# Kernel tuning notes

Measured on AMD Instinct MI355X. Metric: run time of the kernel, lower is better.

Reference implementation:

```python
import jax, jax.numpy as jnp
import numpy as np

N = 8000          # num_nodes
DEG = 8           # avg out-degree of random road graph
B = 32            # batch size
INPUT_DIM = 2
UNITS = 64        # rnn_units
K = 2             # max_diffusion_step
NUM_SUPPORTS = 2  # dual_random_walk


def _spmm(rows, cols, vals, x):
    # sparse @ dense: y[r] += vals * x[c] for each coo entry (r, c)
    return jax.ops.segment_sum(vals[:, None] * x[cols], rows, num_segments=N)


def _gconv(inputs, state, supports, W, b):
    # Chebyshev-style diffusion conv, faithful to GCONV.forward layout
    Bsz = inputs.shape[0]
    x = jnp.concatenate([inputs.reshape(Bsz, N, -1), state.reshape(Bsz, N, -1)], axis=2)
    F = x.shape[2]                                   # input_dim + units
    x0 = jnp.transpose(x, (1, 2, 0)).reshape(N, F * Bsz)
    xs = [x0]
    for rows, cols, vals in supports:
        x1 = _spmm(rows, cols, vals, x0)
        xs.append(x1)
        xk2, xk1 = x0, x1
        for _ in range(2, K + 1):
            x2 = 2.0 * _spmm(rows, cols, vals, xk1) - xk2
            xs.append(x2)
            xk2, xk1 = xk1, x2
    M = len(xs)                                      # num_matrices = 2*K+1
    xc = jnp.stack(xs).reshape(M, N, F, Bsz)
    xc = jnp.transpose(xc, (3, 1, 2, 0)).reshape(Bsz * N, F * M)
    out = xc @ W + b
    return out.reshape(Bsz, N * W.shape[1])


def setup_inputs() -> dict:
    rng = np.random.default_rng(0)
    rows = np.repeat(np.arange(N, dtype=np.int32), DEG)
    cols = rng.integers(0, N, size=N * DEG).astype(np.int32)
    vals = rng.uniform(0.5, 1.5, size=N * DEG).astype(np.float32)
    # random-walk normalization: rw(A) = D^-1 A ; supports are rw(A).T and rw(A.T).T
    rsum = np.zeros(N, np.float32); np.add.at(rsum, rows, vals)
    csum = np.zeros(N, np.float32); np.add.at(csum, cols, vals)
    rinv = np.where(rsum > 0, 1.0 / np.maximum(rsum, 1e-12), 0.0).astype(np.float32)
    cinv = np.where(csum > 0, 1.0 / np.maximum(csum, 1e-12), 0.0).astype(np.float32)
    # support0 = (D^-1 A)^T: entry (cols[i], rows[i]) = vals[i] * rinv[rows[i]]
    s0_rows, s0_cols, s0_vals = cols, rows, (vals * rinv[rows]).astype(np.float32)
    # support1 = (D_T^-1 A^T)^T: entry (rows[i], cols[i]) = vals[i] * cinv[cols[i]]
    s1_rows, s1_cols, s1_vals = rows, cols, (vals * cinv[cols]).astype(np.float32)

    key = jax.random.key(0)
    k1, k2, k3, k4 = jax.random.split(key, 4)
    F = INPUT_DIM + UNITS
    M = NUM_SUPPORTS * K + 1
    xavier = lambda k, shape: jax.random.normal(k, shape, jnp.float32) * np.float32(np.sqrt(2.0 / (shape[0] + shape[1])))
    W_ru = xavier(k1, (F * M, 2 * UNITS))
    b_ru = jnp.ones((2 * UNITS,), jnp.float32)    # bias_start=1.0
    W_c = xavier(k2, (F * M, UNITS))
    b_c = jnp.zeros((UNITS,), jnp.float32)        # bias_start=0.0
    inputs = jax.random.normal(k3, (B, N * INPUT_DIM), jnp.float32)
    hx = jax.random.normal(k4, (B, N * UNITS), jnp.float32)
    return {
        "inputs": inputs, "hx": hx,
        "W_ru": W_ru, "b_ru": b_ru, "W_c": W_c, "b_c": b_c,
        "s0_rows": jnp.asarray(s0_rows), "s0_cols": jnp.asarray(s0_cols), "s0_vals": jnp.asarray(s0_vals),
        "s1_rows": jnp.asarray(s1_rows), "s1_cols": jnp.asarray(s1_cols), "s1_vals": jnp.asarray(s1_vals),
    }


def reference(inputs, hx, W_ru, b_ru, W_c, b_c,
              s0_rows, s0_cols, s0_vals, s1_rows, s1_cols, s1_vals):
    supports = [(s0_rows, s0_cols, s0_vals), (s1_rows, s1_cols, s1_vals)]
    value = jax.nn.sigmoid(_gconv(inputs, hx, supports, W_ru, b_ru))
    value = value.reshape(-1, N, 2 * UNITS)
    r = value[..., :UNITS].reshape(-1, N * UNITS)
    u = value[..., UNITS:].reshape(-1, N * UNITS)
    c = jnp.tanh(_gconv(inputs, r * hx, supports, W_c, b_c))
    return u * hx + (1.0 - u) * c
```

## Files before the change

kernel.cpp:

```cpp
#include <hip/hip_runtime.h>
#include <stdint.h>

typedef unsigned short u16;
typedef unsigned int   u32;

typedef __attribute__((ext_vector_type(8))) short bf16x8;
typedef __attribute__((ext_vector_type(4))) float f32x4;

#define NNODES 8000
#define BSZ    32
#define UNITS  64
#define EDG    64000
#define ROWCH  288
#define ROWU16 2304
#define KLIN   480
#define HXROW  512000
#define INROW  16000
#define NROW   18432000
#define NSTEPS 15

__device__ __forceinline__ u32 f2bf(float f){
    u32 u = __float_as_uint(f);
    return (u + 0x7FFFu + ((u >> 16) & 1u)) >> 16;
}
__device__ __forceinline__ float bfu(u16 s){ return __uint_as_float(((u32)s) << 16); }
__device__ __forceinline__ float lo16(u32 u){ return __uint_as_float(u << 16); }
__device__ __forceinline__ float hi16(u32 u){ return __uint_as_float(u & 0xFFFF0000u); }
__device__ __forceinline__ float sigm(float x){ return 1.f / (1.f + __expf(-x)); }

#define GLDS(gsrc, ldst) \
    __builtin_amdgcn_global_load_lds((const __attribute__((address_space(1))) void*)(gsrc), \
                                     (__attribute__((address_space(3))) void*)(ldst), 16, 0, 0)

__global__ void hist_k(const int* __restrict__ rows, int* __restrict__ counts){
    int e = blockIdx.x * 256 + threadIdx.x;
    if (e < EDG) atomicAdd(&counts[rows[e]], 1);
}

__global__ __launch_bounds__(256) void scan_k(const int* __restrict__ counts,
                                              int* __restrict__ row_ptr,
                                              int* __restrict__ cursor){
    __shared__ int part[256];
    int t = threadIdx.x;
    int s = 0;
    for (int i = 0; i < 32; ++i){ int r = t*32 + i; if (r < NNODES) s += counts[r]; }
    part[t] = s;
    __syncthreads();
    if (t == 0){
        int run = 0;
        for (int i = 0; i < 256; ++i){ int v = part[i]; part[i] = run; run += v; }
    }
    __syncthreads();
    int run = part[t];
    for (int i = 0; i < 32; ++i){
        int r = t*32 + i;
        if (r < NNODES){ row_ptr[r] = run; cursor[r] = run; run += counts[r]; }
    }
    if (t == 255) row_ptr[NNODES] = run;
}

__global__ void scatter_k(const int* __restrict__ rows, const int* __restrict__ cols,
                          const float* __restrict__ vals, int* __restrict__ cursor,
                          int* __restrict__ cs, float* __restrict__ vs){
    int e = blockIdx.x * 256 + threadIdx.x;
    if (e < EDG){
        int r = rows[e];
        int slot = atomicAdd(&cursor[r], 1);
        cs[slot] = cols[e];
        vs[slot] = vals[e];
    }
}

__global__ void prep_w_k(const float* __restrict__ W_ru, const float* __restrict__ W_c,
                         u16* __restrict__ Wt_ru, u16* __restrict__ Wt_c){
    int id = blockIdx.x * 256 + threadIdx.x;
    if (id < 128*KLIN){
        int j = id & 7;
        int cell = id >> 3;
        int col = cell & 127;
        int sq = cell >> 7;
        int kl = sq*8 + j;
        int m = kl / 96, fp = kl - m*96;
        u16 v = 0;
        if (fp < 66) v = (u16)f2bf(W_ru[(fp*5 + m)*128 + col]);
        Wt_ru[id] = v;
    }
    int id2 = id - 128*KLIN;
    if (id2 >= 0 && id2 < 64*KLIN){
        int j = id2 & 7;
        int cell = id2 >> 3;
        int col = cell & 63;
        int sq = cell >> 6;
        int kl = sq*8 + j;
        int m = kl / 96, fp = kl - m*96;
        u16 v = 0;
        if (fp < 66) v = (u16)f2bf(W_c[(fp*5 + m)*64 + col]);
        Wt_c[id2] = v;
    }
}

__global__ __launch_bounds__(256) void build_x0_k(const float* __restrict__ inputs,
                                                  const float* __restrict__ hx,
                                                  u16* __restrict__ X0){
    __shared__ float sl[32*72];
    int n = blockIdx.x, t = threadIdx.x;
    #pragma unroll
    for (int i = 0; i < 8; ++i){
        int idx = t + i*256;
        int b = idx >> 6, f = idx & 63;
        sl[b*72 + 2 + f] = hx[b*HXROW + n*64 + f];
    }
    if (t < 64){
        int b = t >> 1, d = t & 1;
        sl[b*72 + d] = inputs[b*INROW + n*2 + d];
    }
    if (t < 192){
        int b = t / 6, k = t - b*6;
        sl[b*72 + 66 + k] = 0.f;
    }
    __syncthreads();
    #pragma unroll
    for (int i = 0; i < 2; ++i){
        int j = t + i*256;
        if (j < ROWCH){
            int b = j & 31, s = j >> 5;
            const float* p = &sl[b*72 + s*8];
            uint4 o;
            o.x = f2bf(p[0]) | (f2bf(p[1]) << 16);
            o.y = f2bf(p[2]) | (f2bf(p[3]) << 16);
            o.z = f2bf(p[4]) | (f2bf(p[5]) << 16);
            o.w = f2bf(p[6]) | (f2bf(p[7]) << 16);
            ((uint4*)X0)[n*ROWCH + j] = o;
        }
    }
}

__device__ __forceinline__ void acc8(float* a, uint4 q, float v){
    a[0] += v*lo16(q.x); a[1] += v*hi16(q.x);
    a[2] += v*lo16(q.y); a[3] += v*hi16(q.y);
    a[4] += v*lo16(q.z); a[5] += v*hi16(q.z);
    a[6] += v*lo16(q.w); a[7] += v*hi16(q.w);
}
__device__ __forceinline__ uint4 pack8(const float* a){
    uint4 o;
    o.x = f2bf(a[0]) | (f2bf(a[1]) << 16);
    o.y = f2bf(a[2]) | (f2bf(a[3]) << 16);
    o.z = f2bf(a[4]) | (f2bf(a[5]) << 16);
    o.w = f2bf(a[6]) | (f2bf(a[7]) << 16);
    return o;
}

__global__ __launch_bounds__(288) void diff1_k(const u16* __restrict__ X0,
                                               u16* __restrict__ X1a, u16* __restrict__ X1b,
                                               const int* __restrict__ rp,
                                               const int* __restrict__ c0, const float* __restrict__ v0,
                                               const int* __restrict__ c1, const float* __restrict__ v1){
    int t = threadIdx.x;
    if (t >= ROWCH) return;
    int n = blockIdx.x;
    const uint4* xb = (const uint4*)X0;
    float a[8] = {0,0,0,0,0,0,0,0};
    float d[8] = {0,0,0,0,0,0,0,0};
    {
        uint4 q[8]; float vv[8];
        #pragma unroll
        for (int i = 0; i < 8; ++i){
            int c = c1[n*8 + i]; vv[i] = v1[n*8 + i];
            q[i] = xb[(size_t)c*ROWCH + t];
        }
        #pragma unroll
        for (int i = 0; i < 8; ++i) acc8(d, q[i], vv[i]);
    }
    int e = rp[n], end = rp[n+1];
    for (; e + 8 <= end; e += 8){
        uint4 q[8]; float vv[8];
        #pragma unroll
        for (int i = 0; i < 8; ++i){
            int c = c0[e+i]; vv[i] = v0[e+i];
            q[i] = xb[(size_t)c*ROWCH + t];
        }
        #pragma unroll
        for (int i = 0; i < 8; ++i) acc8(a, q[i], vv[i]);
    }
    for (; e < end; ++e){
        int c = c0[e]; float v = v0[e];
        acc8(a, xb[(size_t)c*ROWCH + t], v);
    }
    ((uint4*)X1a)[(size_t)n*ROWCH + t] = pack8(a);
    ((uint4*)X1b)[(size_t)n*ROWCH + t] = pack8(d);
}

__global__ __launch_bounds__(288) void diff2_k(const u16* __restrict__ X0,
                                               const u16* __restrict__ X1a, const u16* __restrict__ X1b,
                                               u16* __restrict__ X2a, u16* __restrict__ X2b,
                                               const int* __restrict__ rp,
                                               const int* __restrict__ c0, const float* __restrict__ v0,
                                               const int* __restrict__ c1, const float* __restrict__ v1){
    int t = threadIdx.x;
    if (t >= ROWCH) return;
    int n = blockIdx.x;
    const uint4* xa = (const uint4*)X1a;
    const uint4* xbb = (const uint4*)X1b;
    uint4 pv = ((const uint4*)X0)[(size_t)n*ROWCH + t];
    float a[8] = {0,0,0,0,0,0,0,0};
    float d[8] = {0,0,0,0,0,0,0,0};
    {
        uint4 q[8]; float vv[8];
        #pragma unroll
        for (int i = 0; i < 8; ++i){
            int c = c1[n*8 + i]; vv[i] = v1[n*8 + i];
            q[i] = xbb[(size_t)c*ROWCH + t];
        }
        #pragma unroll
        for (int i = 0; i < 8; ++i) acc8(d, q[i], vv[i]);
    }
    int e = rp[n], end = rp[n+1];
    for (; e + 8 <= end; e += 8){
        uint4 q[8]; float vv[8];
        #pragma unroll
        for (int i = 0; i < 8; ++i){
            int c = c0[e+i]; vv[i] = v0[e+i];
            q[i] = xa[(size_t)c*ROWCH + t];
        }
        #pragma unroll
        for (int i = 0; i < 8; ++i) acc8(a, q[i], vv[i]);
    }
    for (; e < end; ++e){
        int c = c0[e]; float v = v0[e];
        acc8(a, xa[(size_t)c*ROWCH + t], v);
    }
    float p[8] = { lo16(pv.x), hi16(pv.x), lo16(pv.y), hi16(pv.y),
                   lo16(pv.z), hi16(pv.z), lo16(pv.w), hi16(pv.w) };
    #pragma unroll
    for (int i = 0; i < 8; ++i){ a[i] = 2.f*a[i] - p[i]; d[i] = 2.f*d[i] - p[i]; }
    ((uint4*)X2a)[(size_t)n*ROWCH + t] = pack8(a);
    ((uint4*)X2b)[(size_t)n*ROWCH + t] = pack8(d);
}

__global__ __launch_bounds__(256) void gemm_ru_k(
        const u16* X0, const u16* __restrict__ X1a, const u16* __restrict__ X2a,
        const u16* __restrict__ X1b, const u16* __restrict__ X2b,
        const u16* __restrict__ WtS,
        const float* __restrict__ b_ru,
        u16* __restrict__ U, u16* X0st){
    __shared__ u16 Bs[2][4096];
    const int t = threadIdx.x;
    const int lane = t & 63, w = t >> 6;
    const int node = blockIdx.x*4 + w;
    const int cIn = lane & 15, q = lane >> 4;
    const size_t noff = (size_t)node * ROWU16;

    const u16* xp[5] = { X0 + noff, X1a + noff, X2a + noff, X1b + noff, X2b + noff };

    f32x4 acc[2][8];
    const f32x4 z4 = {0.f,0.f,0.f,0.f};
    #pragma unroll
    for (int rt = 0; rt < 2; ++rt)
        #pragma unroll
        for (int ct = 0; ct < 8; ++ct) acc[rt][ct] = z4;

    {
        const u16* src = WtS + t*8;
        GLDS(src,        &Bs[0][w*512]);
        GLDS(src + 2048, &Bs[0][2048 + w*512]);
    }
    bf16x8 A0 = *(const bf16x8*)&xp[0][(size_t)(q*32 + cIn)*8];
    bf16x8 A1 = *(const bf16x8*)&xp[0][(size_t)(q*32 + 16 + cIn)*8];
    __syncthreads();

    int cur = 0;
    #pragma unroll
    for (int st = 0; st < NSTEPS; ++st){
        bf16x8 p0, p1;
        if (st + 1 < NSTEPS){
            const u16* src = WtS + (size_t)(st+1)*4096 + t*8;
            GLDS(src,        &Bs[cur^1][w*512]);
            GLDS(src + 2048, &Bs[cur^1][2048 + w*512]);
            const int m2 = (st+1)/3, s2 = (st+1) - m2*3;
            p0 = *(const bf16x8*)&xp[m2][(size_t)((s2*4 + q)*32 + cIn)*8];
            p1 = *(const bf16x8*)&xp[m2][(size_t)((s2*4 + q)*32 + 16 + cIn)*8];
        }
        bf16x8 cb[8];
        #pragma unroll
        for (int ct = 0; ct < 8; ++ct)
            cb[ct] = *(const bf16x8*)&Bs[cur][(q*128 + ct*16 + cIn)*8];
        #pragma unroll
        for (int ct = 0; ct < 8; ++ct){
            acc[0][ct] = __builtin_amdgcn_mfma_f32_16x16x32_bf16(A0, cb[ct], acc[0][ct], 0,0,0);
            acc[1][ct] = __builtin_amdgcn_mfma_f32_16x16x32_bf16(A1, cb[ct], acc[1][ct], 0,0,0);
        }
        __syncthreads();
        if (st + 1 < NSTEPS){ A0 = p0; A1 = p1; }
        cur ^= 1;
    }

    #pragma unroll
    for (int ct = 0; ct < 8; ++ct){
        int col = ct*16 + cIn;
        float bias = b_ru[col];
        #pragma unroll
        for (int rt = 0; rt < 2; ++rt){
            int b0 = rt*16 + q*4;
            f32x4 d = acc[rt][ct];
            if (ct < 4){
                int fp = 2 + col;
                int s = fp >> 3, off = fp & 7;
                #pragma unroll
                for (int i = 0; i < 4; ++i){
                    size_t idx = noff + (size_t)(s*32 + b0 + i)*8 + off;
                    float h = bfu(X0st[idx]);
                    float rg = sigm(d[i] + bias);
                    X0st[idx] = (u16)f2bf(rg * h);
                }
            } else {
                uint2 pk;
                float v0 = sigm(d[0] + bias), v1 = sigm(d[1] + bias);
                float v2 = sigm(d[2] + bias), v3 = sigm(d[3] + bias);
                pk.x = f2bf(v0) | (f2bf(v1) << 16);
                pk.y = f2bf(v2) | (f2bf(v3) << 16);
                *(uint2*)&U[(size_t)node*2048 + (col - 64)*32 + b0] = pk;
            }
        }
    }
}

__global__ __launch_bounds__(256) void gemm_c_k(
        const u16* __restrict__ X0, const u16* __restrict__ X1a, const u16* __restrict__ X2a,
        const u16* __restrict__ X1b, const u16* __restrict__ X2b,
        const u16* __restrict__ WtS,
        const float* __restrict__ b_c, const float* __restrict__ hx,
        const u16* __restrict__ U, float* __restrict__ out){
    __shared__ u16 Bs[2][2048];
    const int t = threadIdx.x;
    const int lane = t & 63, w = t >> 6;
    const int node = blockIdx.x*4 + w;
    const int cIn = lane & 15, q = lane >> 4;
    const size_t noff = (size_t)node * ROWU16;

    const u16* xp[5] = { X0 + noff, X1a + noff, X2a + noff, X1b + noff, X2b + noff };

    f32x4 acc[2][4];
    const f32x4 z4 = {0.f,0.f,0.f,0.f};
    #pragma unroll
    for (int rt = 0; rt < 2; ++rt)
        #pragma unroll
        for (int ct = 0; ct < 4; ++ct) acc[rt][ct] = z4;

    {
        const u16* src = WtS + t*8;
        GLDS(src, &Bs[0][w*512]);
    }
    bf16x8 A0 = *(const bf16x8*)&xp[0][(size_t)(q*32 + cIn)*8];
    bf16x8 A1 = *(const bf16x8*)&xp[0][(size_t)(q*32 + 16 + cIn)*8];
    __syncthreads();

    int cur = 0;
    #pragma unroll
    for (int st = 0; st < NSTEPS; ++st){
        bf16x8 p0, p1;
        if (st + 1 < NSTEPS){
            const u16* src = WtS + (size_t)(st+1)*2048 + t*8;
            GLDS(src, &Bs[cur^1][w*512]);
            const int m2 = (st+1)/3, s2 = (st+1) - m2*3;
            p0 = *(const bf16x8*)&xp[m2][(size_t)((s2*4 + q)*32 + cIn)*8];
            p1 = *(const bf16x8*)&xp[m2][(size_t)((s2*4 + q)*32 + 16 + cIn)*8];
        }
        bf16x8 cb[4];
        #pragma unroll
        for (int ct = 0; ct < 4; ++ct)
            cb[ct] = *(const bf16x8*)&Bs[cur][(q*64 + ct*16 + cIn)*8];
        #pragma unroll
        for (int ct = 0; ct < 4; ++ct){
            acc[0][ct] = __builtin_amdgcn_mfma_f32_16x16x32_bf16(A0, cb[ct], acc[0][ct], 0,0,0);
            acc[1][ct] = __builtin_amdgcn_mfma_f32_16x16x32_bf16(A1, cb[ct], acc[1][ct], 0,0,0);
        }
        __syncthreads();
        if (st + 1 < NSTEPS){ A0 = p0; A1 = p1; }
        cur ^= 1;
    }

    #pragma unroll
    for (int ct = 0; ct < 4; ++ct){
        int col = ct*16 + cIn;
        float bias = b_c[col];
        #pragma unroll
        for (int rt = 0; rt < 2; ++rt){
            int b0 = rt*16 + q*4;
            f32x4 d = acc[rt][ct];
            uint2 up = *(const uint2*)&U[(size_t)node*2048 + col*32 + b0];
            float uu[4] = { lo16(up.x), hi16(up.x), lo16(up.y), hi16(up.y) };
            #pragma unroll
            for (int i = 0; i < 4; ++i){
                float c = tanhf(d[i] + bias);
                size_t gi = (size_t)(b0 + i)*HXROW + node*64 + col;
                float h = hx[gi];
                out[gi] = uu[i]*h + (1.f - uu[i])*c;
            }
        }
    }
}

extern "C" void kernel_launch(void* const* d_in, const int* in_sizes, int n_in,
                              void* d_out, int out_size, void* d_ws, size_t ws_size,
                              hipStream_t stream){
    const float* inputs = (const float*)d_in[0];
    const float* hx     = (const float*)d_in[1];
    const float* W_ru   = (const float*)d_in[2];
    const float* b_ru   = (const float*)d_in[3];
    const float* W_c    = (const float*)d_in[4];
    const float* b_c    = (const float*)d_in[5];
    const int*   s0r    = (const int*)d_in[6];
    const int*   s0c    = (const int*)d_in[7];
    const float* s0v    = (const float*)d_in[8];
    const int*   s1c    = (const int*)d_in[10];
    const float* s1v    = (const float*)d_in[11];
    float* out = (float*)d_out;

    char* ws = (char*)d_ws;
    size_t off = 0;
    auto alloc = [&](size_t bytes) -> char* {
        char* p = ws + off;
        off += (bytes + 255) & ~(size_t)255;
        return p;
    };
    const size_t XBYTES = (size_t)NROW*2 + 2048;
    u16* X0   = (u16*)alloc(XBYTES);
    u16* X1a  = (u16*)alloc(XBYTES);
    u16* X2a  = (u16*)alloc(XBYTES);
    u16* X1b  = (u16*)alloc(XBYTES);
    u16* X2b  = (u16*)alloc(XBYTES);
    u16* U    = (u16*)alloc((size_t)NNODES*2048*2);
    u16* WtRU = (u16*)alloc((size_t)128*KLIN*2);
    u16* WtC  = (u16*)alloc((size_t)64*KLIN*2);
    int* counts  = (int*)alloc((size_t)NNODES*4);
    int* row_ptr = (int*)alloc((size_t)(NNODES+1)*4);
    int* cursor  = (int*)alloc((size_t)NNODES*4);
    int*   cols_s = (int*)alloc((size_t)EDG*4);
    float* vals_s = (float*)alloc((size_t)EDG*4);
    (void)ws_size; (void)in_sizes; (void)n_in; (void)out_size;

    hipMemsetAsync(counts, 0, (size_t)NNODES*4, stream);
    hist_k<<<250, 256, 0, stream>>>(s0r, counts);
    scan_k<<<1, 256, 0, stream>>>(counts, row_ptr, cursor);
    scatter_k<<<250, 256, 0, stream>>>(s0r, s0c, s0v, cursor, cols_s, vals_s);

    prep_w_k<<<360, 256, 0, stream>>>(W_ru, W_c, WtRU, WtC);
    build_x0_k<<<NNODES, 256, 0, stream>>>(inputs, hx, X0);

    diff1_k<<<NNODES, 288, 0, stream>>>(X0, X1a, X1b, row_ptr, cols_s, vals_s, s1c, s1v);
    diff2_k<<<NNODES, 288, 0, stream>>>(X0, X1a, X1b, X2a, X2b, row_ptr, cols_s, vals_s, s1c, s1v);

    gemm_ru_k<<<NNODES/4, 256, 0, stream>>>(X0, X1a, X2a, X1b, X2b, WtRU, b_ru, U, X0);

    diff1_k<<<NNODES, 288, 0, stream>>>(X0, X1a, X1b, row_ptr, cols_s, vals_s, s1c, s1v);
    diff2_k<<<NNODES, 288, 0, stream>>>(X0, X1a, X1b, X2a, X2b, row_ptr, cols_s, vals_s, s1c, s1v);

    gemm_c_k<<<NNODES/4, 256, 0, stream>>>(X0, X1a, X2a, X1b, X2b, WtC, b_c, hx, U, out);
}
```

Measured before the change: 671.4 us.

## Pad CSR rows to multiples of eight and software-pipeline diffusion gathers

Each CSR row of support0 is padded to a multiple of eight entries, with padded slots set to column 0 and weight 0, so the scalar tail loop is gone. The diffusion kernels now issue all index loads and gather loads for both supports up front. They also double-buffer the next block of eight gathers while accumulating the current block, to hide gather latency. The cost is higher register use per thread, which may lower occupancy, plus extra zero-weight gathers and two more memsets.

```diff
diff --git a/kernel.cpp b/kernel.cpp
--- a/kernel.cpp
+++ b/kernel.cpp
@@ -11,6 +11,7 @@
 #define BSZ    32
 #define UNITS  64
 #define EDG    64000
+#define EDGPAD 120000
 #define ROWCH  288
 #define ROWU16 2304
 #define KLIN   480
@@ -43,7 +44,7 @@
     __shared__ int part[256];
     int t = threadIdx.x;
     int s = 0;
-    for (int i = 0; i < 32; ++i){ int r = t*32 + i; if (r < NNODES) s += counts[r]; }
+    for (int i = 0; i < 32; ++i){ int r = t*32 + i; if (r < NNODES) s += (counts[r] + 7) & ~7; }
     part[t] = s;
     __syncthreads();
     if (t == 0){
@@ -54,7 +55,7 @@
     int run = part[t];
     for (int i = 0; i < 32; ++i){
         int r = t*32 + i;
-        if (r < NNODES){ row_ptr[r] = run; cursor[r] = run; run += counts[r]; }
+        if (r < NNODES){ row_ptr[r] = run; cursor[r] = run; run += (counts[r] + 7) & ~7; }
     }
     if (t == 255) row_ptr[NNODES] = run;
 }
@@ -156,36 +157,51 @@
                                                const int* __restrict__ c0, const float* __restrict__ v0,
                                                const int* __restrict__ c1, const float* __restrict__ v1){
     int t = threadIdx.x;
-    if (t >= ROWCH) return;
     int n = blockIdx.x;
     const uint4* xb = (const uint4*)X0;
+
+    int cc1[8]; float w1[8];
+    #pragma unroll
+    for (int i = 0; i < 8; ++i){ cc1[i] = c1[n*8 + i]; w1[i] = v1[n*8 + i]; }
+    int e = rp[n];
+    const int nb = (rp[n+1] - e) >> 3;
+    int cc0[8]; float w0[8];
+    if (nb > 0){
+        #pragma unroll
+        for (int i = 0; i < 8; ++i){ cc0[i] = c0[e+i]; w0[i] = v0[e+i]; }
+    }
+    uint4 q1[8];
+    #pragma unroll
+    for (int i = 0; i < 8; ++i) q1[i] = xb[(size_t)cc1[i]*ROWCH + t];
+    uint4 q0[8];
+    if (nb > 0){
+        #pragma unroll
+        for (int i = 0; i < 8; ++i) q0[i] = xb[(size_t)cc0[i]*ROWCH + t];
+    }
+
+    float d[8] = {0,0,0,0,0,0,0,0};
+    #pragma unroll
+    for (int i = 0; i < 8; ++i) acc8(d, q1[i], w1[i]);
+
     float a[8] = {0,0,0,0,0,0,0,0};
-    float d[8] = {0,0,0,0,0,0,0,0};
-    {
-        uint4 q[8]; float vv[8];
-        #pragma unroll
-        for (int i = 0; i < 8; ++i){
-            int c = c1[n*8 + i]; vv[i] = v1[n*8 + i];
-            q[i] = xb[(size_t)c*ROWCH + t];
-        }
-        #pragma unroll
-        for (int i = 0; i < 8; ++i) acc8(d, q[i], vv[i]);
-    }
-    int e = rp[n], end = rp[n+1];
-    for (; e + 8 <= end; e += 8){
-        uint4 q[8]; float vv[8];
-        #pragma unroll
-        for (int i = 0; i < 8; ++i){
-            int c = c0[e+i]; vv[i] = v0[e+i];
-            q[i] = xb[(size_t)c*ROWCH + t];
-        }
-        #pragma unroll
-        for (int i = 0; i < 8; ++i) acc8(a, q[i], vv[i]);
-    }
-    for (; e < end; ++e){
-        int c = c0[e]; float v = v0[e];
-        acc8(a, xb[(size_t)c*ROWCH + t], v);
-    }
+    for (int b = 1; b < nb; ++b){
+        e += 8;
+        int cc2[8]; float w2[8];
+        #pragma unroll
+        for (int i = 0; i < 8; ++i){ cc2[i] = c0[e+i]; w2[i] = v0[e+i]; }
+        uint4 q2[8];
+        #pragma unroll
+        for (int i = 0; i < 8; ++i) q2[i] = xb[(size_t)cc2[i]*ROWCH + t];
+        #pragma unroll
+        for (int i = 0; i < 8; ++i) acc8(a, q0[i], w0[i]);
+        #pragma unroll
+        for (int i = 0; i < 8; ++i){ q0[i] = q2[i]; w0[i] = w2[i]; }
+    }
+    if (nb > 0){
+        #pragma unroll
+        for (int i = 0; i < 8; ++i) acc8(a, q0[i], w0[i]);
+    }
+
     ((uint4*)X1a)[(size_t)n*ROWCH + t] = pack8(a);
     ((uint4*)X1b)[(size_t)n*ROWCH + t] = pack8(d);
 }
@@ -197,38 +213,53 @@
                                                const int* __restrict__ c0, const float* __restrict__ v0,
                                                const int* __restrict__ c1, const float* __restrict__ v1){
     int t = threadIdx.x;
-    if (t >= ROWCH) return;
     int n = blockIdx.x;
-    const uint4* xa = (const uint4*)X1a;
+    const uint4* xa  = (const uint4*)X1a;
     const uint4* xbb = (const uint4*)X1b;
+
+    int cc1[8]; float w1[8];
+    #pragma unroll
+    for (int i = 0; i < 8; ++i){ cc1[i] = c1[n*8 + i]; w1[i] = v1[n*8 + i]; }
+    int e = rp[n];
+    const int nb = (rp[n+1] - e) >> 3;
+    int cc0[8]; float w0[8];
+    if (nb > 0){
+        #pragma unroll
+        for (int i = 0; i < 8; ++i){ cc0[i] = c0[e+i]; w0[i] = v0[e+i]; }
+    }
     uint4 pv = ((const uint4*)X0)[(size_t)n*ROWCH + t];
+    uint4 q1[8];
+    #pragma unroll
+    for (int i = 0; i < 8; ++i) q1[i] = xbb[(size_t)cc1[i]*ROWCH + t];
+    uint4 q0[8];
+    if (nb > 0){
+        #pragma unroll
+        for (int i = 0; i < 8; ++i) q0[i] = xa[(size_t)cc0[i]*ROWCH + t];
+    }
+
+    float d[8] = {0,0,0,0,0,0,0,0};
+    #pragma unroll
+    for (int i = 0; i < 8; ++i) acc8(d, q1[i], w1[i]);
+
     float a[8] = {0,0,0,0,0,0,0,0};
-    float d[8] = {0,0,0,0,0,0,0,0};
-    {
-        uint4 q[8]; float vv[8];
-        #pragma unroll
-        for (int i = 0; i < 8; ++i){
-            int c = c1[n*8 + i]; vv[i] = v1[n*8 + i];
-            q[i] = xbb[(size_t)c*ROWCH + t];
-        }
-        #pragma unroll
-        for (int i = 0; i < 8; ++i) acc8(d, q[i], vv[i]);
-    }
-    int e = rp[n], end = rp[n+1];
-    for (; e + 8 <= end; e += 8){
-        uint4 q[8]; float vv[8];
-        #pragma unroll
-        for (int i = 0; i < 8; ++i){
-            int c = c0[e+i]; vv[i] = v0[e+i];
-            q[i] = xa[(size_t)c*ROWCH + t];
-        }
-        #pragma unroll
-        for (int i = 0; i < 8; ++i) acc8(a, q[i], vv[i]);
-    }
-    for (; e < end; ++e){
-        int c = c0[e]; float v = v0[e];
-        acc8(a, xa[(size_t)c*ROWCH + t], v);
-    }
+    for (int b = 1; b < nb; ++b){
+        e += 8;
+        int cc2[8]; float w2[8];
+        #pragma unroll
+        for (int i = 0; i < 8; ++i){ cc2[i] = c0[e+i]; w2[i] = v0[e+i]; }
+        uint4 q2[8];
+        #pragma unroll
+        for (int i = 0; i < 8; ++i) q2[i] = xa[(size_t)cc2[i]*ROWCH + t];
+        #pragma unroll
+        for (int i = 0; i < 8; ++i) acc8(a, q0[i], w0[i]);
+        #pragma unroll
+        for (int i = 0; i < 8; ++i){ q0[i] = q2[i]; w0[i] = w2[i]; }
+    }
+    if (nb > 0){
+        #pragma unroll
+        for (int i = 0; i < 8; ++i) acc8(a, q0[i], w0[i]);
+    }
+
     float p[8] = { lo16(pv.x), hi16(pv.x), lo16(pv.y), hi16(pv.y),
                    lo16(pv.z), hi16(pv.z), lo16(pv.w), hi16(pv.w) };
     #pragma unroll
@@ -435,11 +466,13 @@
     int* counts  = (int*)alloc((size_t)NNODES*4);
     int* row_ptr = (int*)alloc((size_t)(NNODES+1)*4);
     int* cursor  = (int*)alloc((size_t)NNODES*4);
-    int*   cols_s = (int*)alloc((size_t)EDG*4);
-    float* vals_s = (float*)alloc((size_t)EDG*4);
+    int*   cols_s = (int*)alloc((size_t)EDGPAD*4);
+    float* vals_s = (float*)alloc((size_t)EDGPAD*4);
     (void)ws_size; (void)in_sizes; (void)n_in; (void)out_size;
 
     hipMemsetAsync(counts, 0, (size_t)NNODES*4, stream);
+    hipMemsetAsync(cols_s, 0, (size_t)EDGPAD*4, stream);
+    hipMemsetAsync(vals_s, 0, (size_t)EDGPAD*4, stream);
     hist_k<<<250, 256, 0, stream>>>(s0r, counts);
     scan_k<<<1, 256, 0, stream>>>(counts, row_ptr, cursor);
     scatter_k<<<250, 256, 0, stream>>>(s0r, s0c, s0v, cursor, cols_s, vals_s);
```

Result: slower. 709.0 us (+5.6%).

## Pad CSR rows to multiples of eight and interleave nodes across diffusion blocks

Applied to the files above, without the earlier changes.

Each CSR row of support 0 is padded to a multiple of 8 entries, filled with zero column/value entries, so the diffusion kernels can drop the scalar remainder loop and always run the unrolled 8-wide gather. The diffusion kernels also remap their blocks so each block covers a 36-chunk slice of 8 different nodes instead of the full row of one node. The goal is uniform unrolled loops with more loads in flight, and a different spread of gather traffic. The cost is wasted loads and FMAs on padded entries (up to almost double the edge count) plus extra memsets, and a wave now mixes nodes with different trip counts.

```diff
diff --git a/kernel.cpp b/kernel.cpp
--- a/kernel.cpp
+++ b/kernel.cpp
@@ -11,6 +11,7 @@
 #define BSZ    32
 #define UNITS  64
 #define EDG    64000
+#define EDGPAD 120000
 #define ROWCH  288
 #define ROWU16 2304
 #define KLIN   480
@@ -43,7 +44,7 @@
     __shared__ int part[256];
     int t = threadIdx.x;
     int s = 0;
-    for (int i = 0; i < 32; ++i){ int r = t*32 + i; if (r < NNODES) s += counts[r]; }
+    for (int i = 0; i < 32; ++i){ int r = t*32 + i; if (r < NNODES) s += (counts[r] + 7) & ~7; }
     part[t] = s;
     __syncthreads();
     if (t == 0){
@@ -54,7 +55,7 @@
     int run = part[t];
     for (int i = 0; i < 32; ++i){
         int r = t*32 + i;
-        if (r < NNODES){ row_ptr[r] = run; cursor[r] = run; run += counts[r]; }
+        if (r < NNODES){ row_ptr[r] = run; cursor[r] = run; run += (counts[r] + 7) & ~7; }
     }
     if (t == 255) row_ptr[NNODES] = run;
 }
@@ -155,10 +156,12 @@
                                                const int* __restrict__ rp,
                                                const int* __restrict__ c0, const float* __restrict__ v0,
                                                const int* __restrict__ c1, const float* __restrict__ v1){
-    int t = threadIdx.x;
-    if (t >= ROWCH) return;
-    int n = blockIdx.x;
+    const int sl = blockIdx.x & 7, ng = blockIdx.x >> 3;
+    const int ln = threadIdx.x / 36, j = threadIdx.x - ln*36;
+    const int n = ng*8 + ln;
+    const int t = sl*36 + j;
     const uint4* xb = (const uint4*)X0;
+
     float a[8] = {0,0,0,0,0,0,0,0};
     float d[8] = {0,0,0,0,0,0,0,0};
     {
@@ -172,7 +175,7 @@
         for (int i = 0; i < 8; ++i) acc8(d, q[i], vv[i]);
     }
     int e = rp[n], end = rp[n+1];
-    for (; e + 8 <= end; e += 8){
+    for (; e < end; e += 8){
         uint4 q[8]; float vv[8];
         #pragma unroll
         for (int i = 0; i < 8; ++i){
@@ -181,10 +184,6 @@
         }
         #pragma unroll
         for (int i = 0; i < 8; ++i) acc8(a, q[i], vv[i]);
-    }
-    for (; e < end; ++e){
-        int c = c0[e]; float v = v0[e];
-        acc8(a, xb[(size_t)c*ROWCH + t], v);
     }
     ((uint4*)X1a)[(size_t)n*ROWCH + t] = pack8(a);
     ((uint4*)X1b)[(size_t)n*ROWCH + t] = pack8(d);
@@ -196,11 +195,13 @@
                                                const int* __restrict__ rp,
                                                const int* __restrict__ c0, const float* __restrict__ v0,
                                                const int* __restrict__ c1, const float* __restrict__ v1){
-    int t = threadIdx.x;
-    if (t >= ROWCH) return;
-    int n = blockIdx.x;
-    const uint4* xa = (const uint4*)X1a;
+    const int sl = blockIdx.x & 7, ng = blockIdx.x >> 3;
+    const int ln = threadIdx.x / 36, j = threadIdx.x - ln*36;
+    const int n = ng*8 + ln;
+    const int t = sl*36 + j;
+    const uint4* xa  = (const uint4*)X1a;
     const uint4* xbb = (const uint4*)X1b;
+
     uint4 pv = ((const uint4*)X0)[(size_t)n*ROWCH + t];
     float a[8] = {0,0,0,0,0,0,0,0};
     float d[8] = {0,0,0,0,0,0,0,0};
@@ -215,7 +216,7 @@
         for (int i = 0; i < 8; ++i) acc8(d, q[i], vv[i]);
     }
     int e = rp[n], end = rp[n+1];
-    for (; e + 8 <= end; e += 8){
+    for (; e < end; e += 8){
         uint4 q[8]; float vv[8];
         #pragma unroll
         for (int i = 0; i < 8; ++i){
@@ -224,10 +225,6 @@
         }
         #pragma unroll
         for (int i = 0; i < 8; ++i) acc8(a, q[i], vv[i]);
-    }
-    for (; e < end; ++e){
-        int c = c0[e]; float v = v0[e];
-        acc8(a, xa[(size_t)c*ROWCH + t], v);
     }
     float p[8] = { lo16(pv.x), hi16(pv.x), lo16(pv.y), hi16(pv.y),
                    lo16(pv.z), hi16(pv.z), lo16(pv.w), hi16(pv.w) };
@@ -435,11 +432,13 @@
     int* counts  = (int*)alloc((size_t)NNODES*4);
     int* row_ptr = (int*)alloc((size_t)(NNODES+1)*4);
     int* cursor  = (int*)alloc((size_t)NNODES*4);
-    int*   cols_s = (int*)alloc((size_t)EDG*4);
-    float* vals_s = (float*)alloc((size_t)EDG*4);
+    int*   cols_s = (int*)alloc((size_t)EDGPAD*4);
+    float* vals_s = (float*)alloc((size_t)EDGPAD*4);
     (void)ws_size; (void)in_sizes; (void)n_in; (void)out_size;
 
     hipMemsetAsync(counts, 0, (size_t)NNODES*4, stream);
+    hipMemsetAsync(cols_s, 0, (size_t)EDGPAD*4, stream);
+    hipMemsetAsync(vals_s, 0, (size_t)EDGPAD*4, stream);
     hist_k<<<250, 256, 0, stream>>>(s0r, counts);
     scan_k<<<1, 256, 0, stream>>>(counts, row_ptr, cursor);
     scatter_k<<<250, 256, 0, stream>>>(s0r, s0c, s0v, cursor, cols_s, vals_s);
```

Measured after the change: 671.5 us. No clear change (+0.0%).

## Fold Chebyshev recurrence into weights and widen GEMM blocks to eight nodes

Applied to the files above, without the earlier changes.

The 2*Sx1 - x0 step is moved out of the diffusion kernel by folding it into the weight matrix: the m=0 weight becomes W0-W2-W4 and the m=2 and m=4 weights are doubled, so diff2 only writes the raw second diffusion. This removes a read of X0 per node and the elementwise pass in diff2. Separately, the GEMM kernels now process eight nodes per 512-thread block, sharing each weight tile across more waves. Rounding the combined and scaled weights to bf16 may change numerical error slightly.

```diff
diff --git a/kernel.cpp b/kernel.cpp
--- a/kernel.cpp
+++ b/kernel.cpp
@@ -82,7 +82,14 @@
         int kl = sq*8 + j;
         int m = kl / 96, fp = kl - m*96;
         u16 v = 0;
-        if (fp < 66) v = (u16)f2bf(W_ru[(fp*5 + m)*128 + col]);
+        if (fp < 66){
+            float w;
+            if (m == 0)      w = W_ru[(fp*5 + 0)*128 + col] - W_ru[(fp*5 + 2)*128 + col] - W_ru[(fp*5 + 4)*128 + col];
+            else if (m == 2) w = 2.f * W_ru[(fp*5 + 2)*128 + col];
+            else if (m == 4) w = 2.f * W_ru[(fp*5 + 4)*128 + col];
+            else             w = W_ru[(fp*5 + m)*128 + col];
+            v = (u16)f2bf(w);
+        }
         Wt_ru[id] = v;
     }
     int id2 = id - 128*KLIN;
@@ -94,7 +101,14 @@
         int kl = sq*8 + j;
         int m = kl / 96, fp = kl - m*96;
         u16 v = 0;
-        if (fp < 66) v = (u16)f2bf(W_c[(fp*5 + m)*64 + col]);
+        if (fp < 66){
+            float w;
+            if (m == 0)      w = W_c[(fp*5 + 0)*64 + col] - W_c[(fp*5 + 2)*64 + col] - W_c[(fp*5 + 4)*64 + col];
+            else if (m == 2) w = 2.f * W_c[(fp*5 + 2)*64 + col];
+            else if (m == 4) w = 2.f * W_c[(fp*5 + 4)*64 + col];
+            else             w = W_c[(fp*5 + m)*64 + col];
+            v = (u16)f2bf(w);
+        }
         Wt_c[id2] = v;
     }
 }
@@ -190,9 +204,8 @@
     ((uint4*)X1b)[(size_t)n*ROWCH + t] = pack8(d);
 }
 
-__global__ __launch_bounds__(288) void diff2_k(const u16* __restrict__ X0,
-                                               const u16* __restrict__ X1a, const u16* __restrict__ X1b,
-                                               u16* __restrict__ X2a, u16* __restrict__ X2b,
+__global__ __launch_bounds__(288) void diff2_k(const u16* __restrict__ X1a, const u16* __restrict__ X1b,
+                                               u16* __restrict__ Y2a, u16* __restrict__ Y2b,
                                                const int* __restrict__ rp,
                                                const int* __restrict__ c0, const float* __restrict__ v0,
                                                const int* __restrict__ c1, const float* __restrict__ v1){
@@ -201,7 +214,6 @@
     int n = blockIdx.x;
     const uint4* xa = (const uint4*)X1a;
     const uint4* xbb = (const uint4*)X1b;
-    uint4 pv = ((const uint4*)X0)[(size_t)n*ROWCH + t];
     float a[8] = {0,0,0,0,0,0,0,0};
     float d[8] = {0,0,0,0,0,0,0,0};
     {
@@ -229,15 +241,11 @@
         int c = c0[e]; float v = v0[e];
         acc8(a, xa[(size_t)c*ROWCH + t], v);
     }
-    float p[8] = { lo16(pv.x), hi16(pv.x), lo16(pv.y), hi16(pv.y),
-                   lo16(pv.z), hi16(pv.z), lo16(pv.w), hi16(pv.w) };
-    #pragma unroll
-    for (int i = 0; i < 8; ++i){ a[i] = 2.f*a[i] - p[i]; d[i] = 2.f*d[i] - p[i]; }
-    ((uint4*)X2a)[(size_t)n*ROWCH + t] = pack8(a);
-    ((uint4*)X2b)[(size_t)n*ROWCH + t] = pack8(d);
-}
-
-__global__ __launch_bounds__(256) void gemm_ru_k(
+    ((uint4*)Y2a)[(size_t)n*ROWCH + t] = pack8(a);
+    ((uint4*)Y2b)[(size_t)n*ROWCH + t] = pack8(d);
+}
+
+__global__ __launch_bounds__(512) void gemm_ru_k(
         const u16* X0, const u16* __restrict__ X1a, const u16* __restrict__ X2a,
         const u16* __restrict__ X1b, const u16* __restrict__ X2b,
         const u16* __restrict__ WtS,
@@ -246,7 +254,7 @@
     __shared__ u16 Bs[2][4096];
     const int t = threadIdx.x;
     const int lane = t & 63, w = t >> 6;
-    const int node = blockIdx.x*4 + w;
+    const int node = blockIdx.x*8 + w;
     const int cIn = lane & 15, q = lane >> 4;
     const size_t noff = (size_t)node * ROWU16;
 
@@ -259,11 +267,7 @@
         #pragma unroll
         for (int ct = 0; ct < 8; ++ct) acc[rt][ct] = z4;
 
-    {
-        const u16* src = WtS + t*8;
-        GLDS(src,        &Bs[0][w*512]);
-        GLDS(src + 2048, &Bs[0][2048 + w*512]);
-    }
+    GLDS(WtS + t*8, &Bs[0][w*512]);
     bf16x8 A0 = *(const bf16x8*)&xp[0][(size_t)(q*32 + cIn)*8];
     bf16x8 A1 = *(const bf16x8*)&xp[0][(size_t)(q*32 + 16 + cIn)*8];
     __syncthreads();
@@ -273,9 +277,7 @@
     for (int st = 0; st < NSTEPS; ++st){
         bf16x8 p0, p1;
         if (st + 1 < NSTEPS){
-            const u16* src = WtS + (size_t)(st+1)*4096 + t*8;
-            GLDS(src,        &Bs[cur^1][w*512]);
-            GLDS(src + 2048, &Bs[cur^1][2048 + w*512]);
+            GLDS(WtS + (size_t)(st+1)*4096 + t*8, &Bs[cur^1][w*512]);
             const int m2 = (st+1)/3, s2 = (st+1) - m2*3;
             p0 = *(const bf16x8*)&xp[m2][(size_t)((s2*4 + q)*32 + cIn)*8];
             p1 = *(const bf16x8*)&xp[m2][(size_t)((s2*4 + q)*32 + 16 + cIn)*8];
@@ -324,7 +326,7 @@
     }
 }
 
-__global__ __launch_bounds__(256) void gemm_c_k(
+__global__ __launch_bounds__(512) void gemm_c_k(
         const u16* __restrict__ X0, const u16* __restrict__ X1a, const u16* __restrict__ X2a,
         const u16* __restrict__ X1b, const u16* __restrict__ X2b,
         const u16* __restrict__ WtS,
@@ -333,7 +335,7 @@
     __shared__ u16 Bs[2][2048];
     const int t = threadIdx.x;
     const int lane = t & 63, w = t >> 6;
-    const int node = blockIdx.x*4 + w;
+    const int node = blockIdx.x*8 + w;
     const int cIn = lane & 15, q = lane >> 4;
     const size_t noff = (size_t)node * ROWU16;
 
@@ -346,10 +348,7 @@
         #pragma unroll
         for (int ct = 0; ct < 4; ++ct) acc[rt][ct] = z4;
 
-    {
-        const u16* src = WtS + t*8;
-        GLDS(src, &Bs[0][w*512]);
-    }
+    if (t < 256) GLDS(WtS + t*8, &Bs[0][w*512]);
     bf16x8 A0 = *(const bf16x8*)&xp[0][(size_t)(q*32 + cIn)*8];
     bf16x8 A1 = *(const bf16x8*)&xp[0][(size_t)(q*32 + 16 + cIn)*8];
     __syncthreads();
@@ -359,8 +358,7 @@
     for (int st = 0; st < NSTEPS; ++st){
         bf16x8 p0, p1;
         if (st + 1 < NSTEPS){
-            const u16* src = WtS + (size_t)(st+1)*2048 + t*8;
-            GLDS(src, &Bs[cur^1][w*512]);
+            if (t < 256) GLDS(WtS + (size_t)(st+1)*2048 + t*8, &Bs[cur^1][w*512]);
             const int m2 = (st+1)/3, s2 = (st+1) - m2*3;
             p0 = *(const bf16x8*)&xp[m2][(size_t)((s2*4 + q)*32 + cIn)*8];
             p1 = *(const bf16x8*)&xp[m2][(size_t)((s2*4 + q)*32 + 16 + cIn)*8];
@@ -448,12 +446,12 @@
     build_x0_k<<<NNODES, 256, 0, stream>>>(inputs, hx, X0);
 
     diff1_k<<<NNODES, 288, 0, stream>>>(X0, X1a, X1b, row_ptr, cols_s, vals_s, s1c, s1v);
-    diff2_k<<<NNODES, 288, 0, stream>>>(X0, X1a, X1b, X2a, X2b, row_ptr, cols_s, vals_s, s1c, s1v);
-
-    gemm_ru_k<<<NNODES/4, 256, 0, stream>>>(X0, X1a, X2a, X1b, X2b, WtRU, b_ru, U, X0);
+    diff2_k<<<NNODES, 288, 0, stream>>>(X1a, X1b, X2a, X2b, row_ptr, cols_s, vals_s, s1c, s1v);
+
+    gemm_ru_k<<<NNODES/8, 512, 0, stream>>>(X0, X1a, X2a, X1b, X2b, WtRU, b_ru, U, X0);
 
     diff1_k<<<NNODES, 288, 0, stream>>>(X0, X1a, X1b, row_ptr, cols_s, vals_s, s1c, s1v);
-    diff2_k<<<NNODES, 288, 0, stream>>>(X0, X1a, X1b, X2a, X2b, row_ptr, cols_s, vals_s, s1c, s1v);
-
-    gemm_c_k<<<NNODES/4, 256, 0, stream>>>(X0, X1a, X2a, X1b, X2b, WtC, b_c, hx, U, out);
-}
+    diff2_k<<<NNODES, 288, 0, stream>>>(X1a, X1b, X2a, X2b, row_ptr, cols_s, vals_s, s1c, s1v);
+
+    gemm_c_k<<<NNODES/8, 512, 0, stream>>>(X0, X1a, X2a, X1b, X2b, WtC, b_c, hx, U, out);
+}
```

Measured after the change: 665.4 us. Within noise of the previous version (-0.9%).
